# Kernel tuning notes

Hardware: AMD Instinct MI355X
Metric: run time of the kernel (lower is better)

## Reference

```python
import jax, jax.numpy as jnp
import numpy as np
from jax import lax

B, C, T = 8, 512, 4096
K = 3
DILATIONS = (1, 3, 5)
EPS_Q = 1e-5
EPS_SNAKE = 1e-9


def quantize_weight(w):
    # BitNet-1.58-style ternary quantization with per-tensor absmean scale,
    # applied with a straight-through estimator.
    s = jnp.mean(jnp.abs(w))
    wq = jnp.clip(jnp.round(w / (s + EPS_Q)), -1.0, 1.0) * s
    return w + lax.stop_gradient(wq - w)


def bitconv1d(x, w, b, dilation, padding):
    # x: [B, C, T], w: [Cout, Cin, K], b: [Cout]
    y = lax.conv_general_dilated(
        x, quantize_weight(w),
        window_strides=(1,),
        padding=[(padding, padding)],
        rhs_dilation=(dilation,),
        dimension_numbers=("NCH", "OIH", "NCH"),
    )
    return y + b[None, :, None]


def snake_beta(x, alpha_p, beta_p):
    # log-scale parametrization: alpha = exp(alpha_p), beta = exp(beta_p)
    a = jnp.exp(alpha_p)[None, :, None]
    b = jnp.exp(beta_p)[None, :, None]
    return x + (1.0 / (b + EPS_SNAKE)) * jnp.sin(a * x) ** 2


def setup_inputs() -> dict:
    key = jax.random.key(0)
    ks = jax.random.split(key, 7)
    return {
        "x": jax.random.normal(ks[0], (B, C, T), dtype=jnp.float32),
        "w1": jax.random.normal(ks[1], (3, C, C, K), dtype=jnp.float32) * 0.05,
        "b1": jax.random.normal(ks[2], (3, C), dtype=jnp.float32) * 0.01,
        "alpha": jax.random.normal(ks[3], (3, C), dtype=jnp.float32) * 0.1,
        "beta": jax.random.normal(ks[4], (3, C), dtype=jnp.float32) * 0.1,
        "w2": jax.random.normal(ks[5], (3, C, C, K), dtype=jnp.float32) * 0.05,
        "b2": jax.random.normal(ks[6], (3, C), dtype=jnp.float32) * 0.01,
    }


def reference(x, w1, b1, alpha, beta, w2, b2):
    for i, d in enumerate(DILATIONS):
        pad1 = d * (K - 1) // 2
        h = bitconv1d(x, w1[i], b1[i], dilation=d, padding=pad1)
        h = snake_beta(h, alpha[i], beta[i])
        h = bitconv1d(h, w2[i], b2[i], dilation=1, padding=(K - 1) // 2)
        x = x + h
    return x
```

## Files before the change

kernel.cpp:

```cpp
#include <hip/hip_runtime.h>
#include <math.h>
#include <stdint.h>


constexpr int B_ = 8, C_ = 512, T_ = 4096, K_ = 3;
constexpr int WELEM = C_ * C_ * K_;

typedef __bf16 bf16x8 __attribute__((ext_vector_type(8)));
typedef float f32x4 __attribute__((ext_vector_type(4)));
typedef unsigned short u16x8 __attribute__((ext_vector_type(8)));

constexpr size_t OFF_PART = 0;
constexpr size_t OFF_S = 4096;
constexpr size_t OFF_AE = 8192;
constexpr size_t OFF_IB = 16384;
constexpr size_t OFF_WQ1 = 32768;
constexpr size_t OFF_WQ2 = OFF_WQ1 + (size_t)3 * WELEM * 2;
constexpr size_t OFF_H = OFF_WQ2 + (size_t)3 * WELEM * 2;
constexpr size_t NBCT = (size_t)B_ * C_ * T_;
constexpr size_t OFF_AHI = OFF_H + NBCT * 4;
constexpr size_t OFF_ALO = OFF_AHI + NBCT * 2;
constexpr size_t OFF_BHI = OFF_ALO + NBCT * 2;
constexpr size_t OFF_BLO = OFF_BHI + NBCT * 2;

__device__ inline unsigned short bf16_rne(float v) {
  unsigned int u = __builtin_bit_cast(unsigned int, v);
  unsigned int r = u + 0x7FFFu + ((u >> 16) & 1u);
  return (unsigned short)(r >> 16);
}

__global__ __launch_bounds__(256)
void absmean_partial(const float* __restrict__ w1, const float* __restrict__ w2,
                     float* __restrict__ part) {
  __shared__ float red[256];
  const int t = blockIdx.y;
  const float* src = (t < 3) ? (w1 + (size_t)t * WELEM) : (w2 + (size_t)(t - 3) * WELEM);
  const int base = blockIdx.x * (256 * 32);
  float v = 0.f;
#pragma unroll
  for (int j = 0; j < 32; ++j) v += fabsf(src[base + j * 256 + threadIdx.x]);
  red[threadIdx.x] = v;
  __syncthreads();
  for (int s = 128; s > 0; s >>= 1) {
    if (threadIdx.x < (unsigned)s) red[threadIdx.x] += red[threadIdx.x + s];
    __syncthreads();
  }
  if (threadIdx.x == 0) part[t * 96 + blockIdx.x] = red[0];
}

__global__ __launch_bounds__(128)
void absmean_final(const float* __restrict__ part, float* __restrict__ svec) {
  __shared__ float red[128];
  const int t = blockIdx.x;
  red[threadIdx.x] = (threadIdx.x < 96) ? part[t * 96 + threadIdx.x] : 0.f;
  __syncthreads();
  for (int s = 64; s > 0; s >>= 1) {
    if (threadIdx.x < (unsigned)s) red[threadIdx.x] += red[threadIdx.x + s];
    __syncthreads();
  }
  if (threadIdx.x == 0) svec[t] = red[0] / (float)WELEM;
}

__global__ __launch_bounds__(256)
void quantize_kernel(const float* __restrict__ src, unsigned short* __restrict__ dst,
                     const float* __restrict__ svec, int sbase) {
  const int idx = blockIdx.x * 256 + threadIdx.x;
  const int j = idx & 7;
  const int lane = (idx >> 3) & 63;
  const int cot = (idx >> 9) & 31;
  const int rest = idx >> 14;
  const int tap = rest % 3;
  const int rest2 = rest / 3;
  const int cc = rest2 & 15;
  const int st = rest2 >> 4;
  const int co = cot * 16 + (lane & 15);
  const int ci = cc * 32 + (lane >> 4) * 8 + j;
  const float s = svec[sbase + st];
  const float w = src[(((size_t)st * C_ + co) * C_ + ci) * K_ + tap];
  float q = rintf(w / (s + 1e-5f));
  q = fminf(1.f, fmaxf(-1.f, q));
  dst[idx] = (unsigned short)(__builtin_bit_cast(unsigned int, q) >> 16);
}

__global__ __launch_bounds__(256)
void snake_params_kernel(const float* __restrict__ al, const float* __restrict__ be,
                         float* __restrict__ ae, float* __restrict__ ib) {
  const int idx = blockIdx.x * 256 + threadIdx.x;
  if (idx < 3 * C_) {
    ae[idx] = expf(al[idx]);
    ib[idx] = 1.f / (expf(be[idx]) + 1e-9f);
  }
}

__global__ __launch_bounds__(256)
void transpose_split(const float* __restrict__ X, unsigned short* __restrict__ Hi,
                     unsigned short* __restrict__ Lo) {
  __shared__ float tile[64][68];
  const int b = blockIdx.z;
  const int c0 = blockIdx.y * 64;
  const int t0 = blockIdx.x * 64;
  const int tid = threadIdx.x;
  {
    const int cl = tid >> 2, tg = tid & 3;
    const float* src = X + ((size_t)b * C_ + c0 + cl) * T_ + t0 + tg * 16;
    float4 v0 = *(const float4*)(src);
    float4 v1 = *(const float4*)(src + 4);
    float4 v2 = *(const float4*)(src + 8);
    float4 v3 = *(const float4*)(src + 12);
    float* d = &tile[cl][tg * 16];
    *(float4*)(d) = v0; *(float4*)(d + 4) = v1;
    *(float4*)(d + 8) = v2; *(float4*)(d + 12) = v3;
  }
  __syncthreads();
  {
    const int tl = tid >> 2, cg = tid & 3;
    u16x8 h0, h1, l0, l1;
#pragma unroll
    for (int j = 0; j < 16; ++j) {
      const float v = tile[cg * 16 + j][tl];
      const unsigned short hb = bf16_rne(v);
      const float hf = __builtin_bit_cast(float, (unsigned int)hb << 16);
      const unsigned short lb = bf16_rne(v - hf);
      if (j < 8) { h0[j] = hb; l0[j] = lb; }
      else       { h1[j - 8] = hb; l1[j - 8] = lb; }
    }
    const size_t off = ((size_t)b * T_ + t0 + tl) * C_ + c0 + cg * 16;
    *(u16x8*)(Hi + off) = h0; *(u16x8*)(Hi + off + 8) = h1;
    *(u16x8*)(Lo + off) = l0; *(u16x8*)(Lo + off + 8) = l1;
  }
}

template <int DIL, bool SNAKE>
__global__ __launch_bounds__(256, 2)
void conv_mfma(const unsigned short* __restrict__ Xhi,
               const unsigned short* __restrict__ Xlo,
               const unsigned short* __restrict__ Wq,
               const float* __restrict__ svec,
               const float* __restrict__ bias, const float* __restrict__ aexp,
               const float* __restrict__ invb,
               const float* __restrict__ res,
               float* __restrict__ Y) {
  constexpr int R = 256 + 2 * DIL;
  constexpr int RW = 40;
  __shared__ unsigned short Xs[2][R * RW];

  const int b = blockIdx.z;
  const int co0 = blockIdx.y * 128;
  const int cob = blockIdx.y * 8;
  const int t0 = blockIdx.x * 256;
  const int tid = threadIdx.x;
  const int lane = tid & 63;
  const int wv = tid >> 6;
  const int l15 = lane & 15;
  const int quad = lane >> 4;

  f32x4 acc[8][4] = {};

  const size_t xbase = (size_t)b * T_ * C_;

#pragma unroll 1
  for (int cc = 0; cc < C_ / 32; ++cc) {
    constexpr int XU = R * 8;
#pragma unroll
    for (int it = 0; it < (XU + 255) / 256; ++it) {
      const int u = it * 256 + tid;
      if (u < XU) {
        const int r = u >> 3, sub = u & 7;
        const int pl = sub >> 2, g = sub & 3;
        const int t = t0 - DIL + r;
        u16x8 v = {0, 0, 0, 0, 0, 0, 0, 0};
        if ((unsigned)t < (unsigned)T_)
          v = *(const u16x8*)((pl ? Xlo : Xhi) + xbase + (size_t)t * C_ + cc * 32 + g * 8);
        *(u16x8*)&Xs[pl][r * RW + g * 8] = v;
      }
    }
    __syncthreads();

#pragma unroll 1
    for (int tap = 0; tap < K_; ++tap) {
      const unsigned short* wb =
          Wq + ((((size_t)cc * K_ + tap) * 32 + cob) * 512) + (size_t)lane * 8;
      bf16x8 a[8];
#pragma unroll
      for (int m = 0; m < 8; ++m)
        a[m] = __builtin_bit_cast(bf16x8, *(const u16x8*)(wb + m * 512));
#pragma unroll
      for (int n = 0; n < 4; ++n) {
        const int r = wv * 64 + n * 16 + l15 + tap * DIL;
        const bf16x8 bh = __builtin_bit_cast(bf16x8, *(const u16x8*)&Xs[0][r * RW + quad * 8]);
        const bf16x8 bl = __builtin_bit_cast(bf16x8, *(const u16x8*)&Xs[1][r * RW + quad * 8]);
#pragma unroll
        for (int m = 0; m < 8; ++m) {
          acc[m][n] = __builtin_amdgcn_mfma_f32_16x16x32_bf16(a[m], bh, acc[m][n], 0, 0, 0);
          acc[m][n] = __builtin_amdgcn_mfma_f32_16x16x32_bf16(a[m], bl, acc[m][n], 0, 0, 0);
        }
      }
    }
    __syncthreads();
  }

  const float sw = *svec;
#pragma unroll
  for (int m = 0; m < 8; ++m) {
#pragma unroll
    for (int reg = 0; reg < 4; ++reg) {
      const int co = co0 + m * 16 + quad * 4 + reg;
      const float bs = bias[co];
      float av = 0.f, ibv = 0.f;
      if (SNAKE) { av = aexp[co]; ibv = invb[co]; }
#pragma unroll
      for (int n = 0; n < 4; ++n) {
        const int t = t0 + wv * 64 + n * 16 + l15;
        const size_t off = ((size_t)b * C_ + co) * T_ + t;
        float v = sw * acc[m][n][reg] + bs;
        if (SNAKE) {
          const float sn = __sinf(av * v);
          v = v + ibv * sn * sn;
        } else {
          v = v + res[off];
        }
        Y[off] = v;
      }
    }
  }
}

extern "C" void kernel_launch(void* const* d_in, const int* in_sizes, int n_in,
                              void* d_out, int out_size, void* d_ws, size_t ws_size,
                              hipStream_t stream) {
  (void)in_sizes; (void)n_in; (void)out_size; (void)ws_size;
  const float* x = (const float*)d_in[0];
  const float* w1 = (const float*)d_in[1];
  const float* b1 = (const float*)d_in[2];
  const float* al = (const float*)d_in[3];
  const float* be = (const float*)d_in[4];
  const float* w2 = (const float*)d_in[5];
  const float* b2 = (const float*)d_in[6];
  float* out = (float*)d_out;
  char* wsb = (char*)d_ws;

  float* part = (float*)(wsb + OFF_PART);
  float* svec = (float*)(wsb + OFF_S);
  float* ae = (float*)(wsb + OFF_AE);
  float* ib = (float*)(wsb + OFF_IB);
  unsigned short* wq1 = (unsigned short*)(wsb + OFF_WQ1);
  unsigned short* wq2 = (unsigned short*)(wsb + OFF_WQ2);
  float* h = (float*)(wsb + OFF_H);
  unsigned short* Ahi = (unsigned short*)(wsb + OFF_AHI);
  unsigned short* Alo = (unsigned short*)(wsb + OFF_ALO);
  unsigned short* Bhi = (unsigned short*)(wsb + OFF_BHI);
  unsigned short* Blo = (unsigned short*)(wsb + OFF_BLO);

  absmean_partial<<<dim3(96, 6), 256, 0, stream>>>(w1, w2, part);
  absmean_final<<<6, 128, 0, stream>>>(part, svec);
  quantize_kernel<<<(3 * WELEM) / 256, 256, 0, stream>>>(w1, wq1, svec, 0);
  quantize_kernel<<<(3 * WELEM) / 256, 256, 0, stream>>>(w2, wq2, svec, 3);
  snake_params_kernel<<<6, 256, 0, stream>>>(al, be, ae, ib);

  const dim3 tgrid(T_ / 64, C_ / 64, B_);
  const dim3 cgrid(T_ / 256, C_ / 128, B_);

  transpose_split<<<tgrid, 256, 0, stream>>>(x, Ahi, Alo);

  conv_mfma<1, true><<<cgrid, 256, 0, stream>>>(Ahi, Alo, wq1 + 0 * (size_t)WELEM, svec + 0,
                                                b1 + 0, ae + 0, ib + 0, nullptr, h);
  transpose_split<<<tgrid, 256, 0, stream>>>(h, Bhi, Blo);
  conv_mfma<1, false><<<cgrid, 256, 0, stream>>>(Bhi, Blo, wq2 + 0 * (size_t)WELEM, svec + 3,
                                                 b2 + 0, nullptr, nullptr, x, out);
  transpose_split<<<tgrid, 256, 0, stream>>>(out, Ahi, Alo);

  conv_mfma<3, true><<<cgrid, 256, 0, stream>>>(Ahi, Alo, wq1 + 1 * (size_t)WELEM, svec + 1,
                                                b1 + C_, ae + C_, ib + C_, nullptr, h);
  transpose_split<<<tgrid, 256, 0, stream>>>(h, Bhi, Blo);
  conv_mfma<1, false><<<cgrid, 256, 0, stream>>>(Bhi, Blo, wq2 + 1 * (size_t)WELEM, svec + 4,
                                                 b2 + C_, nullptr, nullptr, out, out);
  transpose_split<<<tgrid, 256, 0, stream>>>(out, Ahi, Alo);

  conv_mfma<5, true><<<cgrid, 256, 0, stream>>>(Ahi, Alo, wq1 + 2 * (size_t)WELEM, svec + 2,
                                                b1 + 2 * C_, ae + 2 * C_, ib + 2 * C_, nullptr, h);
  transpose_split<<<tgrid, 256, 0, stream>>>(h, Bhi, Blo);
  conv_mfma<1, false><<<cgrid, 256, 0, stream>>>(Bhi, Blo, wq2 + 2 * (size_t)WELEM, svec + 5,
                                                 b2 + 2 * C_, nullptr, nullptr, out, out);
}
```

Measured before the change: 870.4 us.

## Fuse bf16 hi/lo plane transpose-split into conv epilogues

The conv epilogue now writes the next conv's input directly as transposed [B,T,C] bf16 hi/lo planes. This removes five standalone transpose_split launches and the fp32 intermediate h buffer. Each such launch cost an extra fp32 read and plane write of the whole activation tensor. The trade-off is narrower 8-byte scattered stores in the epilogue, plus extra rounding work per output element.

```diff
diff --git a/kernel.cpp b/kernel.cpp
--- a/kernel.cpp
+++ b/kernel.cpp
@@ -9,6 +9,7 @@
 typedef __bf16 bf16x8 __attribute__((ext_vector_type(8)));
 typedef float f32x4 __attribute__((ext_vector_type(4)));
 typedef unsigned short u16x8 __attribute__((ext_vector_type(8)));
+typedef unsigned short u16x4 __attribute__((ext_vector_type(4)));
 
 constexpr size_t OFF_PART = 0;
 constexpr size_t OFF_S = 4096;
@@ -16,12 +17,11 @@
 constexpr size_t OFF_IB = 16384;
 constexpr size_t OFF_WQ1 = 32768;
 constexpr size_t OFF_WQ2 = OFF_WQ1 + (size_t)3 * WELEM * 2;
-constexpr size_t OFF_H = OFF_WQ2 + (size_t)3 * WELEM * 2;
 constexpr size_t NBCT = (size_t)B_ * C_ * T_;
-constexpr size_t OFF_AHI = OFF_H + NBCT * 4;
-constexpr size_t OFF_ALO = OFF_AHI + NBCT * 2;
-constexpr size_t OFF_BHI = OFF_ALO + NBCT * 2;
-constexpr size_t OFF_BLO = OFF_BHI + NBCT * 2;
+constexpr size_t OFF_PHI = OFF_WQ2 + (size_t)3 * WELEM * 2;
+constexpr size_t OFF_PLO = OFF_PHI + NBCT * 2;
+constexpr size_t OFF_QHI = OFF_PLO + NBCT * 2;
+constexpr size_t OFF_QLO = OFF_QHI + NBCT * 2;
 
 __device__ inline unsigned short bf16_rne(float v) {
   unsigned int u = __builtin_bit_cast(unsigned int, v);
@@ -130,7 +130,7 @@
   }
 }
 
-template <int DIL, bool SNAKE>
+template <int DIL, bool SNAKE, bool PLANES, bool WF32>
 __global__ __launch_bounds__(256, 2)
 void conv_mfma(const unsigned short* __restrict__ Xhi,
                const unsigned short* __restrict__ Xlo,
@@ -139,7 +139,9 @@
                const float* __restrict__ bias, const float* __restrict__ aexp,
                const float* __restrict__ invb,
                const float* __restrict__ res,
-               float* __restrict__ Y) {
+               float* __restrict__ Y,
+               unsigned short* __restrict__ Ohi,
+               unsigned short* __restrict__ Olo) {
   constexpr int R = 256 + 2 * DIL;
   constexpr int RW = 40;
   __shared__ unsigned short Xs[2][R * RW];
@@ -202,24 +204,41 @@
   const float sw = *svec;
 #pragma unroll
   for (int m = 0; m < 8; ++m) {
+    const int cb = co0 + m * 16 + quad * 4;
+    float bs[4], av[4], ibv[4];
 #pragma unroll
     for (int reg = 0; reg < 4; ++reg) {
-      const int co = co0 + m * 16 + quad * 4 + reg;
-      const float bs = bias[co];
-      float av = 0.f, ibv = 0.f;
-      if (SNAKE) { av = aexp[co]; ibv = invb[co]; }
-#pragma unroll
-      for (int n = 0; n < 4; ++n) {
-        const int t = t0 + wv * 64 + n * 16 + l15;
-        const size_t off = ((size_t)b * C_ + co) * T_ + t;
-        float v = sw * acc[m][n][reg] + bs;
+      bs[reg] = bias[cb + reg];
+      if (SNAKE) { av[reg] = aexp[cb + reg]; ibv[reg] = invb[cb + reg]; }
+    }
+#pragma unroll
+    for (int n = 0; n < 4; ++n) {
+      const int t = t0 + wv * 64 + n * 16 + l15;
+      float vv[4];
+#pragma unroll
+      for (int reg = 0; reg < 4; ++reg) {
+        float v = sw * acc[m][n][reg] + bs[reg];
         if (SNAKE) {
-          const float sn = __sinf(av * v);
-          v = v + ibv * sn * sn;
+          const float sn = __sinf(av[reg] * v);
+          v = v + ibv[reg] * sn * sn;
         } else {
-          v = v + res[off];
+          v = v + res[((size_t)b * C_ + cb + reg) * T_ + t];
         }
-        Y[off] = v;
+        if (WF32) Y[((size_t)b * C_ + cb + reg) * T_ + t] = v;
+        vv[reg] = v;
+      }
+      if (PLANES) {
+        u16x4 hq, lq;
+#pragma unroll
+        for (int reg = 0; reg < 4; ++reg) {
+          const unsigned short hb = bf16_rne(vv[reg]);
+          const float hf = __builtin_bit_cast(float, (unsigned int)hb << 16);
+          hq[reg] = hb;
+          lq[reg] = bf16_rne(vv[reg] - hf);
+        }
+        const size_t poff = ((size_t)b * T_ + t) * C_ + cb;
+        *(u16x4*)(Ohi + poff) = hq;
+        *(u16x4*)(Olo + poff) = lq;
       }
     }
   }
@@ -245,11 +264,10 @@
   float* ib = (float*)(wsb + OFF_IB);
   unsigned short* wq1 = (unsigned short*)(wsb + OFF_WQ1);
   unsigned short* wq2 = (unsigned short*)(wsb + OFF_WQ2);
-  float* h = (float*)(wsb + OFF_H);
-  unsigned short* Ahi = (unsigned short*)(wsb + OFF_AHI);
-  unsigned short* Alo = (unsigned short*)(wsb + OFF_ALO);
-  unsigned short* Bhi = (unsigned short*)(wsb + OFF_BHI);
-  unsigned short* Blo = (unsigned short*)(wsb + OFF_BLO);
+  unsigned short* Phi = (unsigned short*)(wsb + OFF_PHI);
+  unsigned short* Plo = (unsigned short*)(wsb + OFF_PLO);
+  unsigned short* Qhi = (unsigned short*)(wsb + OFF_QHI);
+  unsigned short* Qlo = (unsigned short*)(wsb + OFF_QLO);
 
   absmean_partial<<<dim3(96, 6), 256, 0, stream>>>(w1, w2, part);
   absmean_final<<<6, 128, 0, stream>>>(part, svec);
@@ -260,25 +278,26 @@
   const dim3 tgrid(T_ / 64, C_ / 64, B_);
   const dim3 cgrid(T_ / 256, C_ / 128, B_);
 
-  transpose_split<<<tgrid, 256, 0, stream>>>(x, Ahi, Alo);
-
-  conv_mfma<1, true><<<cgrid, 256, 0, stream>>>(Ahi, Alo, wq1 + 0 * (size_t)WELEM, svec + 0,
-                                                b1 + 0, ae + 0, ib + 0, nullptr, h);
-  transpose_split<<<tgrid, 256, 0, stream>>>(h, Bhi, Blo);
-  conv_mfma<1, false><<<cgrid, 256, 0, stream>>>(Bhi, Blo, wq2 + 0 * (size_t)WELEM, svec + 3,
-                                                 b2 + 0, nullptr, nullptr, x, out);
-  transpose_split<<<tgrid, 256, 0, stream>>>(out, Ahi, Alo);
-
-  conv_mfma<3, true><<<cgrid, 256, 0, stream>>>(Ahi, Alo, wq1 + 1 * (size_t)WELEM, svec + 1,
-                                                b1 + C_, ae + C_, ib + C_, nullptr, h);
-  transpose_split<<<tgrid, 256, 0, stream>>>(h, Bhi, Blo);
-  conv_mfma<1, false><<<cgrid, 256, 0, stream>>>(Bhi, Blo, wq2 + 1 * (size_t)WELEM, svec + 4,
-                                                 b2 + C_, nullptr, nullptr, out, out);
-  transpose_split<<<tgrid, 256, 0, stream>>>(out, Ahi, Alo);
-
-  conv_mfma<5, true><<<cgrid, 256, 0, stream>>>(Ahi, Alo, wq1 + 2 * (size_t)WELEM, svec + 2,
-                                                b1 + 2 * C_, ae + 2 * C_, ib + 2 * C_, nullptr, h);
-  transpose_split<<<tgrid, 256, 0, stream>>>(h, Bhi, Blo);
-  conv_mfma<1, false><<<cgrid, 256, 0, stream>>>(Bhi, Blo, wq2 + 2 * (size_t)WELEM, svec + 5,
-                                                 b2 + 2 * C_, nullptr, nullptr, out, out);
-}
+  transpose_split<<<tgrid, 256, 0, stream>>>(x, Phi, Plo);
+
+  conv_mfma<1, true, true, false><<<cgrid, 256, 0, stream>>>(
+      Phi, Plo, wq1 + 0 * (size_t)WELEM, svec + 0, b1 + 0, ae + 0, ib + 0,
+      nullptr, nullptr, Qhi, Qlo);
+  conv_mfma<1, false, true, true><<<cgrid, 256, 0, stream>>>(
+      Qhi, Qlo, wq2 + 0 * (size_t)WELEM, svec + 3, b2 + 0, nullptr, nullptr,
+      x, out, Phi, Plo);
+
+  conv_mfma<3, true, true, false><<<cgrid, 256, 0, stream>>>(
+      Phi, Plo, wq1 + 1 * (size_t)WELEM, svec + 1, b1 + C_, ae + C_, ib + C_,
+      nullptr, nullptr, Qhi, Qlo);
+  conv_mfma<1, false, true, true><<<cgrid, 256, 0, stream>>>(
+      Qhi, Qlo, wq2 + 1 * (size_t)WELEM, svec + 4, b2 + C_, nullptr, nullptr,
+      out, out, Phi, Plo);
+
+  conv_mfma<5, true, true, false><<<cgrid, 256, 0, stream>>>(
+      Phi, Plo, wq1 + 2 * (size_t)WELEM, svec + 2, b1 + 2 * C_, ae + 2 * C_,
+      ib + 2 * C_, nullptr, nullptr, Qhi, Qlo);
+  conv_mfma<1, false, false, true><<<cgrid, 256, 0, stream>>>(
+      Qhi, Qlo, wq2 + 2 * (size_t)WELEM, svec + 5, b2 + 2 * C_, nullptr, nullptr,
+      out, out, nullptr, nullptr);
+}
```

Result: no change. 860.3 us (-1.2%).
